# Kernel optimization log

Hardware: AMD Instinct MI355X
Metric: run time of the kernel (lower is better)

## Reference

```python
import jax, jax.numpy as jnp
import numpy as np

B, L, D = 8, 8192, 128
H, C = 2, 64          # heads, out_channels = dim // 2; H*C == D so the final view works
N = B * L
E = 1048576
NEG_SLOPE = 0.2


def setup_inputs() -> dict:
    key = jax.random.key(0)
    k1, k2, k3, k4, k5 = jax.random.split(key, 5)
    x = jax.random.normal(k1, (B, L, D), dtype=jnp.float32)
    edge_index = jax.random.randint(k2, (2, E), 0, N, dtype=jnp.int64)
    s = 1.0 / np.sqrt(D)
    W_l = jax.random.uniform(k3, (D, H * C), minval=-s, maxval=s, dtype=jnp.float32)
    W_r = jax.random.uniform(k4, (D, H * C), minval=-s, maxval=s, dtype=jnp.float32)
    att = jax.random.uniform(k5, (H, C), minval=-s, maxval=s, dtype=jnp.float32)
    bias = jnp.zeros((H * C,), dtype=jnp.float32)
    return {"x": x, "edge_index": edge_index, "W_l": W_l, "W_r": W_r, "att": att, "bias": bias}


def reference(x, edge_index, W_l, W_r, att, bias):
    # x: [B, L, D] -> flatten to node features [N, D]
    xf = x.reshape(N, D)
    x_l = (xf @ W_l).reshape(N, H, C)  # source transform
    x_r = (xf @ W_r).reshape(N, H, C)  # target transform

    # add self loops (PyG GATv2Conv default add_self_loops=True)
    loops = jnp.arange(N, dtype=edge_index.dtype)
    src = jnp.concatenate([edge_index[0], loops])  # [E+N]
    dst = jnp.concatenate([edge_index[1], loops])

    # GATv2 attention: e_ij = att . LeakyReLU(x_l[j] + x_r[i])
    feat = jax.nn.leaky_relu(x_l[src] + x_r[dst], NEG_SLOPE)  # [E+N, H, C]
    score = jnp.einsum('ehc,hc->eh', feat, att)               # [E+N, H]

    # segment softmax over incoming edges of each target node
    m = jax.ops.segment_max(score, dst, num_segments=N)       # [N, H]
    num = jnp.exp(score - m[dst])
    den = jax.ops.segment_sum(num, dst, num_segments=N)       # [N, H]
    alpha = num / den[dst]                                    # [E+N, H]

    # weighted aggregation of transformed source features
    out = jax.ops.segment_sum(alpha[:, :, None] * x_l[src], dst, num_segments=N)  # [N, H, C]
    out = out.reshape(N, H * C) + bias
    return out.reshape(B, L, D)
```

## Files before the change

### kernel.cpp

```cpp
#include <hip/hip_runtime.h>

typedef unsigned short u16;
typedef unsigned int   u32;
typedef unsigned long long u64;

#define NN     65536
#define DDIM   128
#define EE     1048576
#define NEG_SLOPE 0.2f
#define SUBCAP 640
#define BROW   8192

typedef __attribute__((ext_vector_type(8))) short          short8;
typedef __attribute__((ext_vector_type(2))) float          f32x2;
typedef __attribute__((ext_vector_type(4))) float          f32x4;
typedef __attribute__((ext_vector_type(4))) u32            u32x4;

__device__ __forceinline__ float bf2f(u16 b) { return __uint_as_float(((u32)b) << 16); }
__device__ __forceinline__ u16 f2bf(float f) {
  u32 u = __float_as_uint(f);
  u += 0x7FFFu + ((u >> 16) & 1u);
  return (u16)(u >> 16);
}
__device__ __forceinline__ f32x2 bfp2f(u32 w) {
  f32x2 r;
  r.x = __uint_as_float(w << 16);
  r.y = __uint_as_float(w & 0xFFFF0000u);
  return r;
}
__device__ __forceinline__ f32x2 pk_max(f32x2 a, f32x2 b) {
  f32x2 r; r.x = fmaxf(a.x, b.x); r.y = fmaxf(a.y, b.y); return r;
}

__global__ __launch_bounds__(256) void pass1_misc(
    const int* __restrict__ ei, u32* __restrict__ cursor,
    u32* __restrict__ subb,
    const float* __restrict__ Wl, const float* __restrict__ Wr,
    u16* __restrict__ wpack)
{
  int b = blockIdx.x, t = threadIdx.x;

  if (b >= 512) {
    int pb = b - 512;
    int colhalf = pb >> 2, ks = pb & 3;
    int lane = t & 63, pp = t >> 6;
    int m16 = lane & 15, quad = lane >> 4;
#pragma unroll
    for (int pq = 0; pq < 2; ++pq) {
      int p = pq * 4 + pp;
      const float* W = (p < 4) ? Wl : Wr;
      int n = colhalf * 64 + (p & 3) * 16 + m16;
#pragma unroll
      for (int j = 0; j < 8; ++j) {
        int k = ks * 32 + quad * 8 + j;
        wpack[(((((colhalf * 4 + ks) * 8) + p) * 64 + lane) * 8) + j] = f2bf(W[k * DDIM + n]);
      }
    }
    return;
  }

  __shared__ u32 lcnt[256];
  __shared__ u32 gb[256];
  __shared__ u32 smd;
  lcnt[t] = 0;
  if (t < 64) {
    int nz = (ei[2 * t + 1] != 0) ? 1 : 0;
    unsigned long long bal = __ballot(nz);
    if (t == 0) smd = (bal == 0ull) ? 1u : 0u;
  }
  __syncthreads();
  u32 md = smd;

  int base = (b * 256 + t) * 8;
  int s[8], d[8];
  if (md) {
    const long long* ei64 = (const long long*)ei;
#pragma unroll
    for (int k = 0; k < 4; ++k) {
      longlong2 sv = *(const longlong2*)(ei64 + base + 2 * k);
      longlong2 dv = *(const longlong2*)(ei64 + EE + base + 2 * k);
      s[2 * k] = (int)sv.x; s[2 * k + 1] = (int)sv.y;
      d[2 * k] = (int)dv.x; d[2 * k + 1] = (int)dv.y;
    }
  } else {
#pragma unroll
    for (int k = 0; k < 2; ++k) {
      int4 sv = *(const int4*)(ei + base + 4 * k);
      int4 dv = *(const int4*)(ei + EE + base + 4 * k);
      s[4 * k] = sv.x; s[4 * k + 1] = sv.y; s[4 * k + 2] = sv.z; s[4 * k + 3] = sv.w;
      d[4 * k] = dv.x; d[4 * k + 1] = dv.y; d[4 * k + 2] = dv.z; d[4 * k + 3] = dv.w;
    }
  }

  u32 rk[8];
#pragma unroll
  for (int e = 0; e < 8; ++e)
    rk[e] = atomicAdd(&lcnt[(u32)d[e] >> 8], 1u);
  __syncthreads();

  int xs = b & 7;
  gb[t] = atomicAdd(&cursor[(t * 8 + xs) * 16], lcnt[t]);
  __syncthreads();

#pragma unroll
  for (int e = 0; e < 8; ++e) {
    u32 cell = (u32)d[e] >> 8;
    u32 pos  = gb[cell] + rk[e];
    if (pos < SUBCAP)
      subb[(size_t)(cell * 8 + xs) * SUBCAP + pos] =
          ((u32)(d[e] & 255) << 16) | (u32)s[e];
  }
}

__device__ __forceinline__ void gemm_body(
    int pb, int tid,
    const float* __restrict__ x, const u16* __restrict__ wpack,
    u16* __restrict__ xl, u16* __restrict__ xr, u16* As)
{
  int wave = tid >> 6;
  int lane = tid & 63;
  int m16  = lane & 15;
  int quad = lane >> 4;
  int mat     = wave >> 1;
  int colhalf = wave & 1;
  int rowbase = pb * 64;

  const u16* wp = wpack + (size_t)colhalf * (4 * 8 * 64 * 8);
  short8 bfr[4][4];
#pragma unroll
  for (int ks = 0; ks < 4; ++ks)
#pragma unroll
    for (int ct = 0; ct < 4; ++ct)
      bfr[ks][ct] = *(const short8*)(wp + ((size_t)(ks * 8 + mat * 4 + ct) * 64 + lane) * 8);

#pragma unroll
  for (int ch = 0; ch < 8; ++ch) {
    int i = ch * 1024 + tid * 4;
    int r = i >> 7, c = i & 127;
    f32x4 v = *(const f32x4*)(x + (size_t)(rowbase + r) * DDIM + c);
    u64 w8 = (u64)f2bf(v[0]) | ((u64)f2bf(v[1]) << 16)
           | ((u64)f2bf(v[2]) << 32) | ((u64)f2bf(v[3]) << 48);
    u32 byte = (u32)(r * 256 + c * 2) ^ ((u32)(r & 7) << 4);
    *(u64*)((char*)As + byte) = w8;
  }
  __syncthreads();

  u16* outp = mat ? xr : xl;
#pragma unroll
  for (int rt = 0; rt < 4; ++rt) {
    int r0 = rowbase + rt * 16;
    f32x4 acc[4] = { {0,0,0,0},{0,0,0,0},{0,0,0,0},{0,0,0,0} };
#pragma unroll
    for (int ks = 0; ks < 4; ++ks) {
      int r = rt * 16 + m16;
      u32 byte = (u32)(r * 256 + ks * 64 + quad * 16) ^ ((u32)(r & 7) << 4);
      short8 a = *(const short8*)((const char*)As + byte);
#pragma unroll
      for (int ct = 0; ct < 4; ++ct)
        acc[ct] = __builtin_amdgcn_mfma_f32_16x16x32_bf16(a, bfr[ks][ct], acc[ct], 0, 0, 0);
    }
#pragma unroll
    for (int ct = 0; ct < 4; ++ct) {
      int c = colhalf * 64 + ct * 16 + m16;
#pragma unroll
      for (int rg = 0; rg < 4; ++rg) {
        int r = r0 + quad * 4 + rg;
        outp[(size_t)r * DDIM + c] = f2bf(acc[ct][rg]);
      }
    }
  }
}

__device__ __forceinline__ void pass2_body(
    int b, int t,
    const u32* __restrict__ cursor, const u32* __restrict__ subb,
    u32* __restrict__ rowptr, u16* __restrict__ csr, u32* __restrict__ perm,
    u32* sh, u32* cnt, u32* cbase, u32* hist)
{
  cnt[t] = 0;
  if (t < 64) hist[t] = 0;
  __syncthreads();

  u32 sizes[8];
#pragma unroll
  for (int x = 0; x < 8; ++x) sizes[x] = min(cursor[(b * 8 + x) * 16], (u32)SUBCAP);

  u32 ent[8][3], rk[8][3];
#pragma unroll
  for (int x = 0; x < 8; ++x) {
    const u32* sp = subb + (size_t)(b * 8 + x) * SUBCAP;
#pragma unroll
    for (int r = 0; r < 3; ++r) {
      u32 i = (u32)t + r * 256u;
      ent[x][r] = 0xFFFFFFFFu; rk[x][r] = 0;
      if (i < sizes[x]) {
        u32 e = sp[i];
        ent[x][r] = e;
        rk[x][r]  = atomicAdd(&cnt[e >> 16], 1u);
      }
    }
  }
  __syncthreads();

  u32 c  = cnt[t];
  u32 dc = min(c, 63u);
  u32 pc = (c + 7u) & ~7u;
  atomicAdd(&hist[dc], 1u);
  sh[t] = pc;
  __syncthreads();
  for (int off = 1; off < 256; off <<= 1) {
    u32 v = sh[t]; u32 a = (t >= off) ? sh[t - off] : 0u;
    __syncthreads(); sh[t] = v + a; __syncthreads();
  }
  u32 loc = sh[t] - pc;
  cbase[t] = loc;
  rowptr[b * 256 + t] = ((b * BROW + loc) << 8) | min(c, 255u);
  __syncthreads();
  if (t == 0) {
    u32 run = 0;
    for (int i = 0; i < 64; ++i) { u32 h = hist[i]; hist[i] = run; run += h; }
  }
  __syncthreads();
  u32 r2 = atomicAdd(&hist[dc], 1u);
  perm[b * 256 + r2] = b * 256 + t;
  __syncthreads();

#pragma unroll
  for (int x = 0; x < 8; ++x)
#pragma unroll
    for (int r = 0; r < 3; ++r)
      if (ent[x][r] != 0xFFFFFFFFu) {
        u32 cell = ent[x][r] >> 16;
        csr[b * BROW + cbase[cell] + rk[x][r]] = (u16)(ent[x][r] & 0xFFFFu);
      }
}

__global__ __launch_bounds__(256) void gemm_pass2(
    const float* __restrict__ x, const u16* __restrict__ wpack,
    u16* __restrict__ xl, u16* __restrict__ xr,
    const u32* __restrict__ cursor, const u32* __restrict__ subb,
    u32* __restrict__ rowptr, u16* __restrict__ csr, u32* __restrict__ perm)
{
  __shared__ u32 smem[4096];
  int b = blockIdx.x;
  if (b < 1024) gemm_body(b, threadIdx.x, x, wpack, xl, xr, (u16*)smem);
  else          pass2_body(b - 1024, threadIdx.x, cursor, subb,
                           rowptr, csr, perm,
                           smem, smem + 256, smem + 512, smem + 768);
}

__device__ __forceinline__ void gat_item(u32x4 xw, const f32x2* av, const f32x2* rv,
                                         float& l, f32x2* acc)
{
  f32x2 xv[4];
  f32x2 sc2 = {0.f, 0.f};
#pragma unroll
  for (int i = 0; i < 4; ++i) {
    xv[i] = bfp2f(xw[i]);
    f32x2 t = xv[i] + rv[i];
    f32x2 lr = pk_max(t, t * NEG_SLOPE);
    sc2 += av[i] * lr;
  }
  float partial = sc2.x + sc2.y;
  partial += __shfl_xor(partial, 1);
  partial += __shfl_xor(partial, 2);
  partial += __shfl_xor(partial, 4);
  float p = __expf(partial);
  l += p;
#pragma unroll
  for (int i = 0; i < 4; ++i) acc[i] += p * xv[i];
}

__global__ __launch_bounds__(256) void gat_fused(
    const u16* __restrict__ xl, const u16* __restrict__ xr,
    const u32* __restrict__ rowptr, const u16* __restrict__ csr,
    const u32* __restrict__ perm,
    const float* __restrict__ att, const float* __restrict__ bias,
    float* __restrict__ out)
{
  int tid    = threadIdx.x;
  int bucket = blockIdx.x & 255;
  int k      = blockIdx.x >> 8;
  int wave   = tid >> 6;
  int wg     = (wave == 0) ? k : (wave == 1) ? (31 - k)
             : (wave == 2) ? (32 + k) : (63 - k);
  int node   = (int)perm[bucket * 256 + wg * 4 + ((tid >> 4) & 3)];
  int q      = tid & 15;
  int c0     = q * 8;
  const u16* __restrict__ xlc = xl + c0;

  u32x4 SW = *(const u32x4*)(xlc + (size_t)node * DDIM);

  f32x2 av[4], rv[4];
  {
    f32x4 a0 = *(const f32x4*)(att + c0);
    f32x4 a1 = *(const f32x4*)(att + c0 + 4);
    av[0].x = a0[0]; av[0].y = a0[1]; av[1].x = a0[2]; av[1].y = a0[3];
    av[2].x = a1[0]; av[2].y = a1[1]; av[3].x = a1[2]; av[3].y = a1[3];
    u32x4 rw = *(const u32x4*)(xr + (size_t)node * DDIM + c0);
#pragma unroll
    for (int i = 0; i < 4; ++i) rv[i] = bfp2f(rw[i]);
  }

  float l = 0.f;
  f32x2 acc[4] = { {0,0},{0,0},{0,0},{0,0} };

  u32 rp  = rowptr[node];
  u32 rs  = rp >> 8;
  int deg = (int)(rp & 255u);
  const u16* __restrict__ cp = csr + rs;

  gat_item(SW, av, rv, l, acc);

  int j = 0;
  while (deg - j >= 16) {
    u32x4 iw0 = *(const u32x4*)(cp + j);
    u32x4 iw1 = *(const u32x4*)(cp + j + 8);
    u32 i0  = iw0.x & 0xFFFFu, i1  = iw0.x >> 16, i2  = iw0.y & 0xFFFFu, i3  = iw0.y >> 16;
    u32 i4  = iw0.z & 0xFFFFu, i5  = iw0.z >> 16, i6  = iw0.w & 0xFFFFu, i7  = iw0.w >> 16;
    u32 i8  = iw1.x & 0xFFFFu, i9  = iw1.x >> 16, i10 = iw1.y & 0xFFFFu, i11 = iw1.y >> 16;
    u32 i12 = iw1.z & 0xFFFFu, i13 = iw1.z >> 16, i14 = iw1.w & 0xFFFFu, i15 = iw1.w >> 16;
    u32x4 L0  = *(const u32x4*)(xlc + (size_t)i0  * DDIM);
    u32x4 L1  = *(const u32x4*)(xlc + (size_t)i1  * DDIM);
    u32x4 L2  = *(const u32x4*)(xlc + (size_t)i2  * DDIM);
    u32x4 L3  = *(const u32x4*)(xlc + (size_t)i3  * DDIM);
    u32x4 L4  = *(const u32x4*)(xlc + (size_t)i4  * DDIM);
    u32x4 L5  = *(const u32x4*)(xlc + (size_t)i5  * DDIM);
    u32x4 L6  = *(const u32x4*)(xlc + (size_t)i6  * DDIM);
    u32x4 L7  = *(const u32x4*)(xlc + (size_t)i7  * DDIM);
    u32x4 L8  = *(const u32x4*)(xlc + (size_t)i8  * DDIM);
    u32x4 L9  = *(const u32x4*)(xlc + (size_t)i9  * DDIM);
    u32x4 L10 = *(const u32x4*)(xlc + (size_t)i10 * DDIM);
    u32x4 L11 = *(const u32x4*)(xlc + (size_t)i11 * DDIM);
    u32x4 L12 = *(const u32x4*)(xlc + (size_t)i12 * DDIM);
    u32x4 L13 = *(const u32x4*)(xlc + (size_t)i13 * DDIM);
    u32x4 L14 = *(const u32x4*)(xlc + (size_t)i14 * DDIM);
    u32x4 L15 = *(const u32x4*)(xlc + (size_t)i15 * DDIM);
    __builtin_amdgcn_sched_barrier(0);
    gat_item(L0,  av, rv, l, acc);
    gat_item(L1,  av, rv, l, acc);
    gat_item(L2,  av, rv, l, acc);
    gat_item(L3,  av, rv, l, acc);
    gat_item(L4,  av, rv, l, acc);
    gat_item(L5,  av, rv, l, acc);
    gat_item(L6,  av, rv, l, acc);
    gat_item(L7,  av, rv, l, acc);
    gat_item(L8,  av, rv, l, acc);
    gat_item(L9,  av, rv, l, acc);
    gat_item(L10, av, rv, l, acc);
    gat_item(L11, av, rv, l, acc);
    gat_item(L12, av, rv, l, acc);
    gat_item(L13, av, rv, l, acc);
    gat_item(L14, av, rv, l, acc);
    gat_item(L15, av, rv, l, acc);
    j += 16;
  }
  if (deg - j >= 8) {
    u32x4 iw = *(const u32x4*)(cp + j);
    u32 i0 = iw.x & 0xFFFFu, i1 = iw.x >> 16, i2 = iw.y & 0xFFFFu, i3 = iw.y >> 16;
    u32 i4 = iw.z & 0xFFFFu, i5 = iw.z >> 16, i6 = iw.w & 0xFFFFu, i7 = iw.w >> 16;
    u32x4 L0 = *(const u32x4*)(xlc + (size_t)i0 * DDIM);
    u32x4 L1 = *(const u32x4*)(xlc + (size_t)i1 * DDIM);
    u32x4 L2 = *(const u32x4*)(xlc + (size_t)i2 * DDIM);
    u32x4 L3 = *(const u32x4*)(xlc + (size_t)i3 * DDIM);
    u32x4 L4 = *(const u32x4*)(xlc + (size_t)i4 * DDIM);
    u32x4 L5 = *(const u32x4*)(xlc + (size_t)i5 * DDIM);
    u32x4 L6 = *(const u32x4*)(xlc + (size_t)i6 * DDIM);
    u32x4 L7 = *(const u32x4*)(xlc + (size_t)i7 * DDIM);
    __builtin_amdgcn_sched_barrier(0);
    gat_item(L0, av, rv, l, acc);
    gat_item(L1, av, rv, l, acc);
    gat_item(L2, av, rv, l, acc);
    gat_item(L3, av, rv, l, acc);
    gat_item(L4, av, rv, l, acc);
    gat_item(L5, av, rv, l, acc);
    gat_item(L6, av, rv, l, acc);
    gat_item(L7, av, rv, l, acc);
    j += 8;
  }
  if (deg - j >= 4) {
    uint2 iw = *(const uint2*)(cp + j);
    u32 i0 = iw.x & 0xFFFFu, i1 = iw.x >> 16, i2 = iw.y & 0xFFFFu, i3 = iw.y >> 16;
    u32x4 L0 = *(const u32x4*)(xlc + (size_t)i0 * DDIM);
    u32x4 L1 = *(const u32x4*)(xlc + (size_t)i1 * DDIM);
    u32x4 L2 = *(const u32x4*)(xlc + (size_t)i2 * DDIM);
    u32x4 L3 = *(const u32x4*)(xlc + (size_t)i3 * DDIM);
    __builtin_amdgcn_sched_barrier(0);
    gat_item(L0, av, rv, l, acc);
    gat_item(L1, av, rv, l, acc);
    gat_item(L2, av, rv, l, acc);
    gat_item(L3, av, rv, l, acc);
    j += 4;
  }
  for (; j < deg; ++j) {
    u32 s = cp[j];
    u32x4 xw = *(const u32x4*)(xlc + (size_t)s * DDIM);
    gat_item(xw, av, rv, l, acc);
  }

  float inv = 1.f / l;
  f32x4 o0, o1;
  o0[0] = fmaf(acc[0].x, inv, bias[c0 + 0]);
  o0[1] = fmaf(acc[0].y, inv, bias[c0 + 1]);
  o0[2] = fmaf(acc[1].x, inv, bias[c0 + 2]);
  o0[3] = fmaf(acc[1].y, inv, bias[c0 + 3]);
  o1[0] = fmaf(acc[2].x, inv, bias[c0 + 4]);
  o1[1] = fmaf(acc[2].y, inv, bias[c0 + 5]);
  o1[2] = fmaf(acc[3].x, inv, bias[c0 + 6]);
  o1[3] = fmaf(acc[3].y, inv, bias[c0 + 7]);
  float* op = out + (size_t)node * DDIM + c0;
  *(f32x4*)op       = o0;
  *(f32x4*)(op + 4) = o1;
}

extern "C" void kernel_launch(void* const* d_in, const int* in_sizes, int n_in,
                              void* d_out, int out_size, void* d_ws, size_t ws_size,
                              hipStream_t stream) {
  (void)in_sizes; (void)n_in; (void)out_size; (void)ws_size;
  const float* x    = (const float*)d_in[0];
  const int*   ei   = (const int*)d_in[1];
  const float* Wl   = (const float*)d_in[2];
  const float* Wr   = (const float*)d_in[3];
  const float* attw = (const float*)d_in[4];
  const float* bias = (const float*)d_in[5];
  float* out = (float*)d_out;

  char* w = (char*)d_ws;
  u16* xl     = (u16*)(w);
  u16* xr     = (u16*)(w + (16u << 20));
  u32* subb   = (u32*)(w + (32u << 20));
  u32* cursor = (u32*)(w + (37u << 20));
  u32* rowptr = (u32*)(w + (37u << 20) + (256u << 10));
  u16* csr    = (u16*)(w + (37u << 20) + (512u << 10));
  u16* wpack  = (u16*)(w + (41u << 20) + (512u << 10));
  u32* perm   = (u32*)(w + (41u << 20) + (640u << 10));

  hipMemsetAsync(cursor, 0, 2048 * 16 * sizeof(u32), stream);
  pass1_misc<<<520, 256, 0, stream>>>(ei, cursor, subb, Wl, Wr, wpack);
  gemm_pass2<<<1280, 256, 0, stream>>>(x, wpack, xl, xr, cursor, subb,
                                       rowptr, csr, perm);
  gat_fused<<<NN / 16, 256, 0, stream>>>(xl, xr, rowptr, csr, perm, attw, bias, out);
}
```

Measured before the change: 166.1 us.

## Replace global-atomic edge binning with per-block fixed-slot buckets and drop memset

Adds a new binning path where each pass1 block writes its edges into private fixed-capacity slots per destination cell, with per-block counts, instead of claiming space through global atomic cursors. This removes the memset launch and the global atomics. Pass2 then walks 512 small slot lists per cell, and CSR placement now uses shared-memory atomic cursors rather than precomputed ranks. The new path is chosen only when the workspace is large enough. Per-block slots are capped at 32 entries, and pass2 reads many short serial lists per thread, which may cost more than the old contiguous reads.

```diff
diff --git a/kernel.cpp b/kernel.cpp
--- a/kernel.cpp
+++ b/kernel.cpp
@@ -9,6 +9,7 @@
 #define EE     1048576
 #define NEG_SLOPE 0.2f
 #define SUBCAP 640
+#define DCAP   32
 #define BROW   8192
 
 typedef __attribute__((ext_vector_type(8))) short          short8;
@@ -32,6 +33,88 @@
   f32x2 r; r.x = fmaxf(a.x, b.x); r.y = fmaxf(a.y, b.y); return r;
 }
 
+__device__ __forceinline__ void wpack_body(int pb, int t,
+    const float* __restrict__ Wl, const float* __restrict__ Wr,
+    u16* __restrict__ wpack)
+{
+  int colhalf = pb >> 2, ks = pb & 3;
+  int lane = t & 63, pp = t >> 6;
+  int m16 = lane & 15, quad = lane >> 4;
+#pragma unroll
+  for (int pq = 0; pq < 2; ++pq) {
+    int p = pq * 4 + pp;
+    const float* W = (p < 4) ? Wl : Wr;
+    int n = colhalf * 64 + (p & 3) * 16 + m16;
+#pragma unroll
+    for (int j = 0; j < 8; ++j) {
+      int k = ks * 32 + quad * 8 + j;
+      wpack[(((((colhalf * 4 + ks) * 8) + p) * 64 + lane) * 8) + j] = f2bf(W[k * DDIM + n]);
+    }
+  }
+}
+
+__device__ __forceinline__ void load_edges8(const int* __restrict__ ei, u32 md,
+                                            int base, int* s, int* d)
+{
+  if (md) {
+    const long long* ei64 = (const long long*)ei;
+#pragma unroll
+    for (int k = 0; k < 4; ++k) {
+      longlong2 sv = *(const longlong2*)(ei64 + base + 2 * k);
+      longlong2 dv = *(const longlong2*)(ei64 + EE + base + 2 * k);
+      s[2 * k] = (int)sv.x; s[2 * k + 1] = (int)sv.y;
+      d[2 * k] = (int)dv.x; d[2 * k + 1] = (int)dv.y;
+    }
+  } else {
+#pragma unroll
+    for (int k = 0; k < 2; ++k) {
+      int4 sv = *(const int4*)(ei + base + 4 * k);
+      int4 dv = *(const int4*)(ei + EE + base + 4 * k);
+      s[4 * k] = sv.x; s[4 * k + 1] = sv.y; s[4 * k + 2] = sv.z; s[4 * k + 3] = sv.w;
+      d[4 * k] = dv.x; d[4 * k + 1] = dv.y; d[4 * k + 2] = dv.z; d[4 * k + 3] = dv.w;
+    }
+  }
+}
+
+__global__ __launch_bounds__(256) void pass1_det(
+    const int* __restrict__ ei, u32* __restrict__ subb2, u16* __restrict__ cnt,
+    const float* __restrict__ Wl, const float* __restrict__ Wr,
+    u16* __restrict__ wpack)
+{
+  int b = blockIdx.x, t = threadIdx.x;
+  if (b >= 512) { wpack_body(b - 512, t, Wl, Wr, wpack); return; }
+
+  __shared__ u32 lcnt[256];
+  __shared__ u32 smd;
+  lcnt[t] = 0;
+  if (t < 64) {
+    int nz = (ei[2 * t + 1] != 0) ? 1 : 0;
+    unsigned long long bal = __ballot(nz);
+    if (t == 0) smd = (bal == 0ull) ? 1u : 0u;
+  }
+  __syncthreads();
+  u32 md = smd;
+
+  int s[8], d[8];
+  load_edges8(ei, md, (b * 256 + t) * 8, s, d);
+
+  u32 rk[8];
+#pragma unroll
+  for (int e = 0; e < 8; ++e)
+    rk[e] = atomicAdd(&lcnt[(u32)d[e] >> 8], 1u);
+  __syncthreads();
+
+  cnt[b * 256 + t] = (u16)min(lcnt[t], (u32)DCAP);
+
+#pragma unroll
+  for (int e = 0; e < 8; ++e) {
+    u32 cell = (u32)d[e] >> 8;
+    if (rk[e] < (u32)DCAP)
+      subb2[((size_t)cell * 512 + b) * DCAP + rk[e]] =
+          ((u32)(d[e] & 255) << 16) | (u32)s[e];
+  }
+}
+
 __global__ __launch_bounds__(256) void pass1_misc(
     const int* __restrict__ ei, u32* __restrict__ cursor,
     u32* __restrict__ subb,
@@ -39,25 +122,7 @@
     u16* __restrict__ wpack)
 {
   int b = blockIdx.x, t = threadIdx.x;
-
-  if (b >= 512) {
-    int pb = b - 512;
-    int colhalf = pb >> 2, ks = pb & 3;
-    int lane = t & 63, pp = t >> 6;
-    int m16 = lane & 15, quad = lane >> 4;
-#pragma unroll
-    for (int pq = 0; pq < 2; ++pq) {
-      int p = pq * 4 + pp;
-      const float* W = (p < 4) ? Wl : Wr;
-      int n = colhalf * 64 + (p & 3) * 16 + m16;
-#pragma unroll
-      for (int j = 0; j < 8; ++j) {
-        int k = ks * 32 + quad * 8 + j;
-        wpack[(((((colhalf * 4 + ks) * 8) + p) * 64 + lane) * 8) + j] = f2bf(W[k * DDIM + n]);
-      }
-    }
-    return;
-  }
+  if (b >= 512) { wpack_body(b - 512, t, Wl, Wr, wpack); return; }
 
   __shared__ u32 lcnt[256];
   __shared__ u32 gb[256];
@@ -71,26 +136,8 @@
   __syncthreads();
   u32 md = smd;
 
-  int base = (b * 256 + t) * 8;
   int s[8], d[8];
-  if (md) {
-    const long long* ei64 = (const long long*)ei;
-#pragma unroll
-    for (int k = 0; k < 4; ++k) {
-      longlong2 sv = *(const longlong2*)(ei64 + base + 2 * k);
-      longlong2 dv = *(const longlong2*)(ei64 + EE + base + 2 * k);
-      s[2 * k] = (int)sv.x; s[2 * k + 1] = (int)sv.y;
-      d[2 * k] = (int)dv.x; d[2 * k + 1] = (int)dv.y;
-    }
-  } else {
-#pragma unroll
-    for (int k = 0; k < 2; ++k) {
-      int4 sv = *(const int4*)(ei + base + 4 * k);
-      int4 dv = *(const int4*)(ei + EE + base + 4 * k);
-      s[4 * k] = sv.x; s[4 * k + 1] = sv.y; s[4 * k + 2] = sv.z; s[4 * k + 3] = sv.w;
-      d[4 * k] = dv.x; d[4 * k + 1] = dv.y; d[4 * k + 2] = dv.z; d[4 * k + 3] = dv.w;
-    }
-  }
+  load_edges8(ei, md, (b * 256 + t) * 8, s, d);
 
   u32 rk[8];
 #pragma unroll
@@ -171,13 +218,76 @@
   }
 }
 
+__device__ __forceinline__ void pass2_scan(
+    int b, int t, u32* sh, u32* cntl, u32* cbase, u32* hist,
+    u32* __restrict__ rowptr, u32* __restrict__ perm)
+{
+  u32 c  = cntl[t];
+  u32 dc = min(c, 63u);
+  u32 pc = (c + 7u) & ~7u;
+  atomicAdd(&hist[dc], 1u);
+  sh[t] = pc;
+  __syncthreads();
+  for (int off = 1; off < 256; off <<= 1) {
+    u32 v = sh[t]; u32 a = (t >= off) ? sh[t - off] : 0u;
+    __syncthreads(); sh[t] = v + a; __syncthreads();
+  }
+  u32 loc = sh[t] - pc;
+  cbase[t] = loc;
+  rowptr[b * 256 + t] = ((b * BROW + loc) << 8) | min(c, 255u);
+  __syncthreads();
+  if (t == 0) {
+    u32 run = 0;
+    for (int i = 0; i < 64; ++i) { u32 h = hist[i]; hist[i] = run; run += h; }
+  }
+  __syncthreads();
+  u32 r2 = atomicAdd(&hist[dc], 1u);
+  perm[b * 256 + r2] = b * 256 + t;
+  __syncthreads();
+}
+
+__device__ __forceinline__ void pass2_body_det(
+    int b, int t,
+    const u32* __restrict__ subb2, const u16* __restrict__ cnt,
+    u32* __restrict__ rowptr, u16* __restrict__ csr, u32* __restrict__ perm,
+    u32* sh, u32* cntl, u32* cbase, u32* hist)
+{
+  cntl[t] = 0;
+  if (t < 64) hist[t] = 0;
+  __syncthreads();
+
+#pragma unroll
+  for (int h = 0; h < 2; ++h) {
+    int blk = t + h * 256;
+    u32 c = cnt[blk * 256 + b];
+    const u32* sp = subb2 + ((size_t)b * 512 + blk) * DCAP;
+    for (u32 p = 0; p < c; ++p)
+      atomicAdd(&cntl[sp[p] >> 16], 1u);
+  }
+  __syncthreads();
+
+  pass2_scan(b, t, sh, cntl, cbase, hist, rowptr, perm);
+
+#pragma unroll
+  for (int h = 0; h < 2; ++h) {
+    int blk = t + h * 256;
+    u32 c = cnt[blk * 256 + b];
+    const u32* sp = subb2 + ((size_t)b * 512 + blk) * DCAP;
+    for (u32 p = 0; p < c; ++p) {
+      u32 e = sp[p];
+      u32 pos = atomicAdd(&cbase[e >> 16], 1u);
+      csr[b * BROW + pos] = (u16)(e & 0xFFFFu);
+    }
+  }
+}
+
 __device__ __forceinline__ void pass2_body(
     int b, int t,
     const u32* __restrict__ cursor, const u32* __restrict__ subb,
     u32* __restrict__ rowptr, u16* __restrict__ csr, u32* __restrict__ perm,
-    u32* sh, u32* cnt, u32* cbase, u32* hist)
-{
-  cnt[t] = 0;
+    u32* sh, u32* cntl, u32* cbase, u32* hist)
+{
+  cntl[t] = 0;
   if (t < 64) hist[t] = 0;
   __syncthreads();
 
@@ -196,34 +306,13 @@
       if (i < sizes[x]) {
         u32 e = sp[i];
         ent[x][r] = e;
-        rk[x][r]  = atomicAdd(&cnt[e >> 16], 1u);
+        rk[x][r]  = atomicAdd(&cntl[e >> 16], 1u);
       }
     }
   }
   __syncthreads();
 
-  u32 c  = cnt[t];
-  u32 dc = min(c, 63u);
-  u32 pc = (c + 7u) & ~7u;
-  atomicAdd(&hist[dc], 1u);
-  sh[t] = pc;
-  __syncthreads();
-  for (int off = 1; off < 256; off <<= 1) {
-    u32 v = sh[t]; u32 a = (t >= off) ? sh[t - off] : 0u;
-    __syncthreads(); sh[t] = v + a; __syncthreads();
-  }
-  u32 loc = sh[t] - pc;
-  cbase[t] = loc;
-  rowptr[b * 256 + t] = ((b * BROW + loc) << 8) | min(c, 255u);
-  __syncthreads();
-  if (t == 0) {
-    u32 run = 0;
-    for (int i = 0; i < 64; ++i) { u32 h = hist[i]; hist[i] = run; run += h; }
-  }
-  __syncthreads();
-  u32 r2 = atomicAdd(&hist[dc], 1u);
-  perm[b * 256 + r2] = b * 256 + t;
-  __syncthreads();
+  pass2_scan(b, t, sh, cntl, cbase, hist, rowptr, perm);
 
 #pragma unroll
   for (int x = 0; x < 8; ++x)
@@ -231,8 +320,23 @@
     for (int r = 0; r < 3; ++r)
       if (ent[x][r] != 0xFFFFFFFFu) {
         u32 cell = ent[x][r] >> 16;
-        csr[b * BROW + cbase[cell] + rk[x][r]] = (u16)(ent[x][r] & 0xFFFFu);
+        u32 pos = atomicAdd(&cbase[cell], 1u);
+        csr[b * BROW + pos] = (u16)(ent[x][r] & 0xFFFFu);
       }
+}
+
+__global__ __launch_bounds__(256) void gemm_pass2_det(
+    const float* __restrict__ x, const u16* __restrict__ wpack,
+    u16* __restrict__ xl, u16* __restrict__ xr,
+    const u32* __restrict__ subb2, const u16* __restrict__ cnt,
+    u32* __restrict__ rowptr, u16* __restrict__ csr, u32* __restrict__ perm)
+{
+  __shared__ u32 smem[4096];
+  int b = blockIdx.x;
+  if (b < 1024) gemm_body(b, threadIdx.x, x, wpack, xl, xr, (u16*)smem);
+  else          pass2_body_det(b - 1024, threadIdx.x, subb2, cnt,
+                               rowptr, csr, perm,
+                               smem, smem + 256, smem + 512, smem + 768);
 }
 
 __global__ __launch_bounds__(256) void gemm_pass2(
@@ -416,7 +520,7 @@
 extern "C" void kernel_launch(void* const* d_in, const int* in_sizes, int n_in,
                               void* d_out, int out_size, void* d_ws, size_t ws_size,
                               hipStream_t stream) {
-  (void)in_sizes; (void)n_in; (void)out_size; (void)ws_size;
+  (void)in_sizes; (void)n_in; (void)out_size;
   const float* x    = (const float*)d_in[0];
   const int*   ei   = (const int*)d_in[1];
   const float* Wl   = (const float*)d_in[2];
@@ -426,18 +530,35 @@
   float* out = (float*)d_out;
 
   char* w = (char*)d_ws;
-  u16* xl     = (u16*)(w);
-  u16* xr     = (u16*)(w + (16u << 20));
-  u32* subb   = (u32*)(w + (32u << 20));
-  u32* cursor = (u32*)(w + (37u << 20));
-  u32* rowptr = (u32*)(w + (37u << 20) + (256u << 10));
-  u16* csr    = (u16*)(w + (37u << 20) + (512u << 10));
-  u16* wpack  = (u16*)(w + (41u << 20) + (512u << 10));
-  u32* perm   = (u32*)(w + (41u << 20) + (640u << 10));
-
-  hipMemsetAsync(cursor, 0, 2048 * 16 * sizeof(u32), stream);
-  pass1_misc<<<520, 256, 0, stream>>>(ei, cursor, subb, Wl, Wr, wpack);
-  gemm_pass2<<<1280, 256, 0, stream>>>(x, wpack, xl, xr, cursor, subb,
-                                       rowptr, csr, perm);
-  gat_fused<<<NN / 16, 256, 0, stream>>>(xl, xr, rowptr, csr, perm, attw, bias, out);
-}
+  u16* xl = (u16*)(w);
+  u16* xr = (u16*)(w + (16u << 20));
+
+  if (ws_size >= (54ull << 20)) {
+    u32* subb2  = (u32*)(w + (32u << 20));
+    u16* cnt    = (u16*)(w + (48u << 20));
+    u32* rowptr = (u32*)(w + (48u << 20) + (512u << 10));
+    u16* csr    = (u16*)(w + (49u << 20));
+    u16* wpack  = (u16*)(w + (53u << 20));
+    u32* perm   = (u32*)(w + (53u << 20) + (128u << 10));
+
+    pass1_det<<<520, 256, 0, stream>>>(ei, subb2, cnt, Wl, Wr, wpack);
+    gemm_pass2_det<<<1280, 256, 0, stream>>>(x, wpack, xl, xr, subb2, cnt,
+                                             rowptr, csr, perm);
+    gat_fused<<<NN / 16, 256, 0, stream>>>(xl, xr, rowptr, csr, perm,
+                                           attw, bias, out);
+  } else {
+    u32* subb   = (u32*)(w + (32u << 20));
+    u32* cursor = (u32*)(w + (37u << 20));
+    u32* rowptr = (u32*)(w + (37u << 20) + (256u << 10));
+    u16* csr    = (u16*)(w + (37u << 20) + (512u << 10));
+    u16* wpack  = (u16*)(w + (41u << 20) + (512u << 10));
+    u32* perm   = (u32*)(w + (41u << 20) + (640u << 10));
+
+    hipMemsetAsync(cursor, 0, 2048 * 16 * sizeof(u32), stream);
+    pass1_misc<<<520, 256, 0, stream>>>(ei, cursor, subb, Wl, Wr, wpack);
+    gemm_pass2<<<1280, 256, 0, stream>>>(x, wpack, xl, xr, cursor, subb,
+                                         rowptr, csr, perm);
+    gat_fused<<<NN / 16, 256, 0, stream>>>(xl, xr, rowptr, csr, perm,
+                                           attw, bias, out);
+  }
+}
```

After: 169.1 us. Within noise of the previous version (+1.8%).
